# Kernel optimization log

Measured on AMD Instinct MI355X. Metric: run time of the kernel, lower is better.

Reference implementation:

```python
import jax, jax.numpy as jnp
import numpy as np
from jax import lax

L = 25            # max_delay (250 // init_spike_step=10, odd)
SIG = 12.0        # max_delay // 2, frozen (requires_grad=False)
BN_EPS = 1e-5
EPS = 1e-7


def _dcls_kernel(W, P):
    # Gaussian interpolation of kernel_count=1 weights onto a dense kernel of size L.
    # W, P: (out, in). Returns (out, in, L).
    grid = jnp.arange(L, dtype=W.dtype) - L // 2          # (L,)
    K = jnp.exp(-0.5 * ((grid[None, None, :] - P[:, :, None]) / SIG) ** 2)
    K = K / (jnp.sum(K, axis=-1, keepdims=True) + EPS)    # normalize over kernel taps
    return W[:, :, None] * K


def _dcls_conv(x_tbc, W, P):
    # x_tbc: (T, B, Cin) -> causal dilated-kernel conv over time -> (T, B, Cout)
    kernel = _dcls_kernel(W, P)                           # (Cout, Cin, L)
    xb = jnp.transpose(x_tbc, (1, 2, 0))                  # (B, Cin, T)
    xb = jnp.pad(xb, ((0, 0), (0, 0), (L - 1, 0)))        # left (causal) padding
    y = lax.conv_general_dilated(xb, kernel, window_strides=(1,), padding='VALID',
                                 dimension_numbers=('NCH', 'OIH', 'NCH'))
    return jnp.transpose(y, (2, 0, 1))                    # (T, B, Cout)


def _bn(x_tbc, gamma, beta):
    # BatchNorm1d with step_mode='m': stats over merged (T, B) per channel.
    mean = jnp.mean(x_tbc, axis=(0, 1))
    var = jnp.var(x_tbc, axis=(0, 1))
    xhat = (x_tbc - mean) * lax.rsqrt(var + BN_EPS)
    return gamma * xhat + beta


def setup_inputs() -> dict:
    key = jax.random.key(0)
    ks = jax.random.split(key, 8)
    B, T, C = 128, 100, 700
    x = jax.random.uniform(ks[0], (B, T, C), dtype=jnp.float32)
    pmax = float(L // 2)
    W1 = jax.random.normal(ks[1], (256, 700), jnp.float32) * (1.0 / np.sqrt(700))
    P1 = jax.random.uniform(ks[2], (256, 700), jnp.float32, minval=-pmax, maxval=pmax)
    W2 = jax.random.normal(ks[3], (256, 256), jnp.float32) * (1.0 / np.sqrt(256))
    P2 = jax.random.uniform(ks[4], (256, 256), jnp.float32, minval=-pmax, maxval=pmax)
    W3 = jax.random.normal(ks[5], (20, 256), jnp.float32) * (1.0 / np.sqrt(256))
    P3 = jax.random.uniform(ks[6], (20, 256), jnp.float32, minval=-pmax, maxval=pmax)
    return {
        'x': x, 'W1': W1, 'P1': P1, 'W2': W2, 'P2': P2, 'W3': W3, 'P3': P3,
        'gamma1': jnp.ones((256,), jnp.float32), 'beta1': jnp.zeros((256,), jnp.float32),
        'gamma2': jnp.ones((256,), jnp.float32), 'beta2': jnp.zeros((256,), jnp.float32),
    }


def reference(x, W1, P1, W2, P2, W3, P3, gamma1, beta1, gamma2, beta2):
    h = jnp.transpose(x, (1, 0, 2))            # (T, B, C)
    h = _dcls_conv(h, W1, P1)                  # (T, B, 256)
    h = jax.nn.relu(_bn(h, gamma1, beta1))     # dropout = identity (eval)
    h = _dcls_conv(h, W2, P2)                  # (T, B, 256)
    h = jax.nn.relu(_bn(h, gamma2, beta2))
    h = _dcls_conv(h, W3, P3)                  # (T, B, 20)
    return jnp.sum(jax.nn.softmax(h, axis=2), axis=0)   # (B, 20)
```

## Files before the change

### kernel.cpp

```cpp
#include <hip/hip_runtime.h>
#include <stdint.h>


#define T_LEN 100
#define B_SZ  128
#define M_ROWS 12800
#define R_RANK 4
#define K_FIR 448

typedef __bf16 v8bf __attribute__((ext_vector_type(8)));
typedef float  v4f  __attribute__((ext_vector_type(4)));
typedef unsigned int uint32;
typedef unsigned short ushort_t;

struct PhiT { float v[25][R_RANK]; };
constexpr double cexp_(double x) {
  double s = 1.0, t = 1.0;
  for (int n = 1; n < 30; ++n) { t = t * x / n; s += t; }
  return s;
}
constexpr PhiT make_phi() {
  PhiT P{};
  for (int tau = 0; tau < 25; ++tau) {
    double u = (tau - 12) / 12.0;
    double g = cexp_(-0.5 * u * u);
    double T0 = 1.0, T1 = u;
    P.v[tau][0] = (float)(g * T0);
    P.v[tau][1] = (float)(g * T1);
    for (int r = 2; r < R_RANK; ++r) {
      double T2 = 2.0 * u * T1 - T0;
      P.v[tau][r] = (float)(g * T2);
      T0 = T1; T1 = T2;
    }
  }
  return P;
}
constexpr PhiT PHI = make_phi();

struct FirNeed { bool v[14][7]; };
constexpr FirNeed make_fir_need() {
  FirNeed f{};
  for (int j = 0; j < 14; ++j)
    for (int a = 0; a < 7; ++a) {
      bool need = false;
      for (int k = 32 * j; k < 32 * j + 32; ++k) {
        if (k >= 400) continue;
        int sd = k % 100;
        if (sd >= 16 * a - 24 && sd <= 16 * a + 15) need = true;
      }
      f.v[j][a] = need;
    }
  return f;
}
constexpr FirNeed FIRNEED = make_fir_need();

__device__ __forceinline__ void gl_lds16(const void* g, void* l) {
  __builtin_amdgcn_global_load_lds(
      (const __attribute__((address_space(1))) char*)g,
      (__attribute__((address_space(3))) char*)l, 16, 0, 0);
}

__device__ __forceinline__ void build_wr_body(
    const float* __restrict__ W, const float* __restrict__ P,
    __bf16* __restrict__ Wr, int CIN, int CINP, int COUT, int COUTP, int o) {
  for (int i = threadIdx.x; i < CINP; i += blockDim.x) {
    bool valid = (o < COUT) && (i < CIN);
    float w = valid ? W[(size_t)o * CIN + i] : 0.f;
    float p = valid ? P[(size_t)o * CIN + i] : 0.f;
    float S = 0.f;
#pragma unroll
    for (int l = 0; l < 25; ++l) {
      float d = ((float)(l - 12) - p) * (1.f / 12.f);
      S += expf(-0.5f * d * d);
    }
    float v = p * (1.f / 12.f);
    float g = w * expf(-0.5f * v * v) / (S + 1e-7f);
    float h = 0.5f * v, hh = h * h;
    float pw = 1.f;
#pragma unroll
    for (int r = 0; r < R_RANK; ++r) {
      float term = pw, sum = pw;
#pragma unroll
      for (int m = 1; m <= 6; ++m) {
        term *= hh / (float)(m * (m + r));
        sum += term;
      }
      float c = g * ((r == 0) ? 1.f : 2.f) * sum;
      Wr[((size_t)r * COUTP + o) * CINP + i] = (__bf16)c;
      pw *= h / (float)(r + 1);
    }
  }
}

__global__ void setup_all(const float* __restrict__ x,
                          const float* __restrict__ W1, const float* __restrict__ P1,
                          const float* __restrict__ W2, const float* __restrict__ P2,
                          const float* __restrict__ W3, const float* __restrict__ P3,
                          __bf16* __restrict__ Xb, __bf16* __restrict__ Wr1,
                          __bf16* __restrict__ Wr2, __bf16* __restrict__ Wr3,
                          __bf16* __restrict__ Af, float* __restrict__ stats) {
  int blk = blockIdx.x;
  if (blk < 256) { build_wr_body(W1, P1, Wr1, 700, 704, 256, 256, blk); return; }
  blk -= 256;
  if (blk < 256) { build_wr_body(W2, P2, Wr2, 256, 256, 256, 256, blk); return; }
  blk -= 256;
  if (blk < 32) { build_wr_body(W3, P3, Wr3, 256, 256, 20, 32, blk); return; }
  blk -= 32;
  if (blk < 196) {
    int idx = blk * 256 + threadIdx.x;
    if (idx < 112 * 448) {
      int t = idx / 448, k = idx - t * 448;
      float v = 0.f;
      if (t < 100 && k < 400) {
        int r = k / 100, s = k - r * 100;
        int tau = s - t + 24;
        if (tau >= 0 && tau < 25) v = PHI.v[tau][r];
      }
      Af[idx] = (__bf16)v;
    }
    return;
  }
  blk -= 196;
  if (blk < 2200) {
    int c0 = blk * 1024 + threadIdx.x;
#pragma unroll
    for (int k = 0; k < 4; ++k) {
      int c = c0 + k * 256;
      int row = c / 176, col4 = c - row * 176;
      int t = row >> 7, b = row & 127;
      uint2 pk;
      __bf16* pb = (__bf16*)&pk;
      if (col4 < 175) {
        const float* src = x + ((size_t)b * T_LEN + t) * 700 + col4 * 4;
        float4 v = *(const float4*)src;
        pb[0] = (__bf16)v.x; pb[1] = (__bf16)v.y;
        pb[2] = (__bf16)v.z; pb[3] = (__bf16)v.w;
      } else {
        pk.x = 0u; pk.y = 0u;
      }
      *(uint2*)&Xb[(size_t)row * 704 + col4 * 4] = pk;
    }
    return;
  }
  blk -= 2200;
  if (blk == 0) {
    for (int i = threadIdx.x; i < 1024; i += 256) stats[i] = 0.f;
  }
}

template <int CINP, int BLK_N, int WROWS, int WCOLS, int CO_SH>
__global__ __launch_bounds__(256, 2)
void gemm_rk64(const __bf16* __restrict__ A, const __bf16* __restrict__ Bm,
               __bf16* __restrict__ Z) {
  constexpr int COUTP = 1 << CO_SH;
  constexpr int WM = 128 / WROWS;
  constexpr int WN = BLK_N / WCOLS;
  constexpr int RM = WM / 16;
  constexpr int RN = WN / 16;
  __shared__ __align__(16) __bf16 sA[128 * 64];
  __shared__ __align__(16) __bf16 sB[BLK_N * 64];

  const int tid = threadIdx.x;
  const int w = tid >> 6, lane = tid & 63;
  const int q = lane >> 4, ln = lane & 15;
  const int wrow = w / WCOLS, wcol = w % WCOLS;
  const int srow8 = lane >> 3;
  const int s8 = lane & 7;

  const int t0 = blockIdx.x;
  const int oc = blockIdx.y * BLK_N;
  const __bf16* Abase = A + (size_t)t0 * 128 * CINP;
  const __bf16* Bbase = Bm + (size_t)oc * CINP;

  v4f acc[RM][RN];
#pragma unroll
  for (int a = 0; a < RM; ++a)
#pragma unroll
    for (int b = 0; b < RN; ++b) acc[a][b] = v4f{0.f, 0.f, 0.f, 0.f};

  for (int ic = 0; ic < CINP; ic += 64) {
    for (int j = w; j < 16; j += 4) {
      int m = j * 8 + srow8;
      int g = s8 ^ (m & 7);
      gl_lds16(Abase + (size_t)m * CINP + ic + g * 8, &sA[j * 512]);
    }
    for (int j = w; j < BLK_N / 8; j += 4) {
      int n = j * 8 + srow8;
      int g = s8 ^ (n & 7);
      gl_lds16(Bbase + (size_t)n * CINP + ic + g * 8, &sB[j * 512]);
    }
    __syncthreads();

#pragma unroll
    for (int s = 0; s < 2; ++s) {
      v8bf af[RM], bfr[RN];
#pragma unroll
      for (int a = 0; a < RM; ++a) {
        int m = wrow * WM + a * 16 + ln;
        af[a] = *(const v8bf*)&sA[m * 64 + ((((s << 2) | q) ^ (m & 7)) * 8)];
      }
#pragma unroll
      for (int b = 0; b < RN; ++b) {
        int n = wcol * WN + b * 16 + ln;
        bfr[b] = *(const v8bf*)&sB[n * 64 + ((((s << 2) | q) ^ (n & 7)) * 8)];
      }
#pragma unroll
      for (int a = 0; a < RM; ++a)
#pragma unroll
        for (int b = 0; b < RN; ++b)
          acc[a][b] = __builtin_amdgcn_mfma_f32_16x16x32_bf16(af[a], bfr[b], acc[a][b], 0, 0, 0);
    }
    __syncthreads();
  }

#pragma unroll
  for (int a = 0; a < RM; ++a) {
#pragma unroll
    for (int b = 0; b < RN; ++b) {
      int n = oc + wcol * WN + b * 16 + ln;
      int r = n >> CO_SH, o = n & (COUTP - 1);
#pragma unroll
      for (int rr = 0; rr < 4; ++rr) {
        int m = t0 * 128 + wrow * WM + a * 16 + q * 4 + rr;
        Z[((size_t)r * M_ROWS + m) * COUTP + o] = (__bf16)acc[a][b][rr];
      }
    }
  }
}

template <int COUTP, bool STATS, bool SOFTMAX>
__global__ __launch_bounds__(256, 2)
void fir_gemm64(const __bf16* __restrict__ Af, const __bf16* __restrict__ Z,
                __bf16* __restrict__ Yout, float* __restrict__ stats,
                float* __restrict__ outp, int N) {
  __shared__ __align__(16) unsigned char smem[46592];

  const int tid = threadIdx.x;
  const int w = tid >> 6, lane = tid & 63;
  const int q = lane >> 4, ln = lane & 15;
  const int srow8 = lane >> 3, s8 = lane & 7;
  const int kp = tid >> 3;
  const int noct = tid & 7;
  const int nb = blockIdx.x * 64;

  v4f acc[7];
#pragma unroll
  for (int a = 0; a < 7; ++a) acc[a] = v4f{0.f, 0.f, 0.f, 0.f};

  uint4 r0, r1;

#define SA_BUF(b) ((__bf16*)(smem + (b) * 23296))
#define SB_BUF(b) ((uint32*)(smem + (b) * 23296 + 14336))

  {
    __bf16* sA = SA_BUF(0);
    for (int j = w; j < 14; j += 4) {
      int m = j * 8 + srow8;
      int g = s8 ^ (m & 7);
      gl_lds16(Af + (size_t)m * K_FIR + 0 + g * 8, &sA[j * 512]);
    }
    const __bf16* zp = Z + (size_t)(0 + kp * 2) * N + nb + noct * 8;
    r0 = *(const uint4*)zp;
    r1 = *(const uint4*)(zp + N);
  }

#pragma unroll
  for (int i = 0; i < 7; ++i) {
    const int cb = i & 1;
    asm volatile("s_waitcnt vmcnt(0)" ::: "memory");
    {
      uint32* sBu = SB_BUF(cb);
      const ushort_t* p0 = (const ushort_t*)&r0;
      const ushort_t* p1 = (const ushort_t*)&r1;
#pragma unroll
      for (int j = 0; j < 8; ++j) {
        uint32 val = (uint32)p0[j] | ((uint32)p1[j] << 16);
        sBu[(noct * 8 + j) * 35 + kp] = val;
      }
    }
    if (i < 6) {
      int kc = (i + 1) * 64;
      __bf16* sA = SA_BUF(cb ^ 1);
      for (int j = w; j < 14; j += 4) {
        int m = j * 8 + srow8;
        int g = s8 ^ (m & 7);
        gl_lds16(Af + (size_t)m * K_FIR + kc + g * 8, &sA[j * 512]);
      }
      const __bf16* zp = Z + (size_t)(kc + kp * 2) * N + nb + noct * 8;
      r0 = *(const uint4*)zp;
      r1 = *(const uint4*)(zp + N);
    }
    asm volatile("s_waitcnt lgkmcnt(0)" ::: "memory");
    __builtin_amdgcn_s_barrier();

    {
      __bf16* sA = SA_BUF(cb);
      uint32* sBu = SB_BUF(cb);
#pragma unroll
      for (int s = 0; s < 2; ++s) {
        v8bf af[7];
#pragma unroll
        for (int a = 0; a < 7; ++a) {
          if (FIRNEED.v[2 * i + s][a]) {
            int m = a * 16 + ln;
            af[a] = *(const v8bf*)&sA[m * 64 + ((((s << 2) | q) ^ (m & 7)) * 8)];
          }
        }
        int base = (w * 16 + ln) * 35 + s * 16 + q * 4;
        uint32 tmp[4] = {sBu[base], sBu[base + 1], sBu[base + 2], sBu[base + 3]};
        v8bf bfr = *(const v8bf*)tmp;
#pragma unroll
        for (int a = 0; a < 7; ++a) {
          if (FIRNEED.v[2 * i + s][a])
            acc[a] = __builtin_amdgcn_mfma_f32_16x16x32_bf16(af[a], bfr, acc[a], 0, 0, 0);
        }
      }
    }
    __builtin_amdgcn_s_barrier();
  }

  int ng = nb + w * 16 + ln;
  if (!SOFTMAX) {
    float s = 0.f, ss = 0.f;
#pragma unroll
    for (int a = 0; a < 7; ++a) {
#pragma unroll
      for (int rr = 0; rr < 4; ++rr) {
        int t = a * 16 + q * 4 + rr;
        float v = acc[a][rr];
        if (t < 100) {
          Yout[(size_t)t * N + ng] = (__bf16)v;
          s += v; ss += v * v;
        }
      }
    }
    if (STATS) {
      s += __shfl_xor(s, 16); ss += __shfl_xor(ss, 16);
      s += __shfl_xor(s, 32); ss += __shfl_xor(ss, 32);
      if (q == 0) {
        int o = ng & (COUTP - 1);
        atomicAdd(&stats[o], s);
        atomicAdd(&stats[COUTP + o], ss);
      }
    }
  } else {
    float* smx = (float*)smem;
    float* lacc = (float*)(smem + 26000);
    int col = w * 16 + ln;
#pragma unroll
    for (int a = 0; a < 7; ++a) {
#pragma unroll
      for (int rr = 0; rr < 4; ++rr) {
        int t = a * 16 + q * 4 + rr;
        if (t < 100) smx[t * 65 + col] = acc[a][rr];
      }
    }
    if (tid < 64) lacc[tid & 63] = 0.f;
    __syncthreads();
    if (tid < 200) {
      int bl = tid / 100, t = tid - bl * 100;
      const float* rr = &smx[t * 65 + bl * 32];
      float v[20], m = -1e30f;
#pragma unroll
      for (int o = 0; o < 20; ++o) { v[o] = rr[o]; m = fmaxf(m, v[o]); }
      float sum = 0.f;
#pragma unroll
      for (int o = 0; o < 20; ++o) { v[o] = expf(v[o] - m); sum += v[o]; }
      float inv = 1.f / sum;
#pragma unroll
      for (int o = 0; o < 20; ++o) atomicAdd(&lacc[bl * 20 + o], v[o] * inv);
    }
    __syncthreads();
    if (tid < 40) {
      int bl = tid / 20, o = tid - bl * 20;
      int b = (nb >> 5) + bl;
      outp[b * 20 + o] = lacc[bl * 20 + o];
    }
  }
#undef SA_BUF
#undef SB_BUF
}

__global__ __launch_bounds__(256)
void bn_apply_relu8(__bf16* __restrict__ h, const float* __restrict__ stats,
                    const float* __restrict__ gamma, const float* __restrict__ beta) {
  int idx = blockIdx.x * 256 + threadIdx.x;
  int co = (idx & 31) * 8;
  size_t row = (size_t)(idx >> 5);
  __bf16* p = h + row * 256 + co;
  uint4 raw = *(const uint4*)p;
  const ushort_t* pr = (const ushort_t*)&raw;
  uint4 outv;
  ushort_t* po = (ushort_t*)&outv;
#pragma unroll
  for (int j = 0; j < 8; ++j) {
    int c = co + j;
    float mean = stats[c] * (1.f / 12800.f);
    float var = stats[256 + c] * (1.f / 12800.f) - mean * mean;
    float inv = rsqrtf(var + 1e-5f) * gamma[c];
    uint32 u = (uint32)pr[j] << 16;
    float xv; __builtin_memcpy(&xv, &u, 4);
    float v = (xv - mean) * inv + beta[c];
    v = fmaxf(v, 0.f);
    __bf16 bv = (__bf16)v;
    po[j] = *(const ushort_t*)&bv;
  }
  *(uint4*)p = outv;
}


extern "C" void kernel_launch(void* const* d_in, const int* in_sizes, int n_in,
                              void* d_out, int out_size, void* d_ws, size_t ws_size,
                              hipStream_t stream) {
  const float* x  = (const float*)d_in[0];
  const float* W1 = (const float*)d_in[1];
  const float* P1 = (const float*)d_in[2];
  const float* W2 = (const float*)d_in[3];
  const float* P2 = (const float*)d_in[4];
  const float* W3 = (const float*)d_in[5];
  const float* P3 = (const float*)d_in[6];
  const float* g1 = (const float*)d_in[7];
  const float* b1 = (const float*)d_in[8];
  const float* g2 = (const float*)d_in[9];
  const float* b2 = (const float*)d_in[10];
  float* out = (float*)d_out;

  constexpr size_t XB_B  = (size_t)M_ROWS * 704 * 2;
  constexpr size_t Z_B   = (size_t)K_FIR * 32768 * 2;
  constexpr size_t Y12_B = (size_t)M_ROWS * 256 * 2;
  constexpr size_t W1_B  = (size_t)R_RANK * 256 * 704 * 2;
  constexpr size_t W2_B  = (size_t)R_RANK * 256 * 256 * 2;
  constexpr size_t W3_B  = (size_t)R_RANK * 32 * 256 * 2;
  constexpr size_t AF_B  = (size_t)112 * K_FIR * 2;
  constexpr size_t ST_B  = 4096;
  constexpr size_t TOTAL = XB_B + Z_B + Y12_B + W1_B + W2_B + W3_B + AF_B + ST_B;
  if (ws_size < TOTAL) return;

  char* ws = (char*)d_ws;
  size_t off = 0;
  __bf16* Xb   = (__bf16*)(ws + off); off += XB_B;
  __bf16* Zb   = (__bf16*)(ws + off); off += Z_B;
  __bf16* Yb   = (__bf16*)(ws + off); off += Y12_B;
  __bf16* Wr1  = (__bf16*)(ws + off); off += W1_B;
  __bf16* Wr2  = (__bf16*)(ws + off); off += W2_B;
  __bf16* Wr3  = (__bf16*)(ws + off); off += W3_B;
  __bf16* Afir = (__bf16*)(ws + off); off += AF_B;
  float*  stats1 = (float*)(ws + off);
  float*  stats2 = stats1 + 512;

  setup_all<<<dim3(2941), 256, 0, stream>>>(x, W1, P1, W2, P2, W3, P3,
                                            Xb, Wr1, Wr2, Wr3, Afir, stats1);

  gemm_rk64<704, 256, 2, 2, 8><<<dim3(100, 4), 256, 0, stream>>>(Xb, Wr1, Zb);
  fir_gemm64<256, true, false><<<dim3(512), 256, 0, stream>>>(
      Afir, Zb, Yb, stats1, nullptr, 32768);
  bn_apply_relu8<<<dim3(1600), 256, 0, stream>>>(Yb, stats1, g1, b1);

  gemm_rk64<256, 256, 2, 2, 8><<<dim3(100, 4), 256, 0, stream>>>(Yb, Wr2, Zb);
  fir_gemm64<256, true, false><<<dim3(512), 256, 0, stream>>>(
      Afir, Zb, Yb, stats2, nullptr, 32768);
  bn_apply_relu8<<<dim3(1600), 256, 0, stream>>>(Yb, stats2, g2, b2);

  gemm_rk64<256, 64, 2, 2, 5><<<dim3(100, 2), 256, 0, stream>>>(Yb, Wr3, Zb);
  fir_gemm64<32, false, true><<<dim3(64), 256, 0, stream>>>(
      Afir, Zb, nullptr, nullptr, out, 4096);
}
```

Baseline: 185.5 us.

## Add 32-column FIR GEMM kernel with finer sparsity skipping for layers 1-2

```diff
diff --git a/kernel.cpp b/kernel.cpp
--- a/kernel.cpp
+++ b/kernel.cpp
@@ -53,6 +53,24 @@
   return f;
 }
 constexpr FirNeed FIRNEED = make_fir_need();
+
+struct FirNeed8 { bool v[14][8]; };
+constexpr FirNeed8 make_fir_need8() {
+  FirNeed8 f{};
+  for (int j = 0; j < 14; ++j)
+    for (int a = 0; a < 8; ++a) {
+      bool need = false;
+      for (int t = 16 * a; t < 16 * a + 16 && t < 100; ++t)
+        for (int k = 32 * j; k < 32 * j + 32; ++k) {
+          if (k >= 400) continue;
+          int sd = k % 100;
+          if (sd >= t - 24 && sd <= t) need = true;
+        }
+      f.v[j][a] = need;
+    }
+  return f;
+}
+constexpr FirNeed8 FIRNEED8 = make_fir_need8();
 
 __device__ __forceinline__ void gl_lds16(const void* g, void* l) {
   __builtin_amdgcn_global_load_lds(
@@ -228,6 +246,122 @@
   }
 }
 
+template <int MH>
+__device__ __forceinline__ void fir32_comp(const __bf16* sA, const uint32* sBu,
+                                           v4f acc[4], int i, int nh, int q, int ln) {
+#pragma unroll
+  for (int s = 0; s < 2; ++s) {
+    int base = (nh * 16 + ln) * 35 + s * 16 + q * 4;
+    uint32 tmp[4] = {sBu[base], sBu[base + 1], sBu[base + 2], sBu[base + 3]};
+    v8bf bfr = *(const v8bf*)tmp;
+#pragma unroll
+    for (int a = 0; a < 4; ++a) {
+      if (FIRNEED8.v[2 * i + s][MH * 4 + a]) {
+        int m = (MH * 4 + a) * 16 + ln;
+        v8bf af = *(const v8bf*)&sA[m * 64 + ((((s << 2) | q) ^ (m & 7)) * 8)];
+        acc[a] = __builtin_amdgcn_mfma_f32_16x16x32_bf16(af, bfr, acc[a], 0, 0, 0);
+      }
+    }
+  }
+}
+
+template <int COUTP>
+__global__ __launch_bounds__(256, 4)
+void fir_gemm32(const __bf16* __restrict__ Af, const __bf16* __restrict__ Z,
+                __bf16* __restrict__ Yout, float* __restrict__ stats, int N) {
+  __shared__ __align__(16) unsigned char smem[37632];
+
+  const int tid = threadIdx.x;
+  const int w = tid >> 6, lane = tid & 63;
+  const int q = lane >> 4, ln = lane & 15;
+  const int srow8 = lane >> 3, s8 = lane & 7;
+  const int kp = tid >> 3;
+  const int noct = tid & 7;
+  const int mh = w >> 1, nh = w & 1;
+  const int nb = blockIdx.x * 32;
+
+  v4f acc[4];
+#pragma unroll
+  for (int a = 0; a < 4; ++a) acc[a] = v4f{0.f, 0.f, 0.f, 0.f};
+
+  uint2 r0, r1;
+
+#define SA32(b) ((__bf16*)(smem + (b) * 18816))
+#define SB32(b) ((uint32*)(smem + (b) * 18816 + 14336))
+
+  {
+    __bf16* sA = SA32(0);
+    for (int j = w; j < 14; j += 4) {
+      int m = j * 8 + srow8;
+      int g = s8 ^ (m & 7);
+      gl_lds16(Af + (size_t)m * K_FIR + 0 + g * 8, &sA[j * 512]);
+    }
+    const __bf16* zp = Z + (size_t)(kp * 2) * N + nb + noct * 4;
+    r0 = *(const uint2*)zp;
+    r1 = *(const uint2*)(zp + N);
+  }
+
+#pragma unroll
+  for (int i = 0; i < 7; ++i) {
+    const int cb = i & 1;
+    asm volatile("s_waitcnt vmcnt(0)" ::: "memory");
+    {
+      uint32* sBu = SB32(cb);
+      const ushort_t* p0 = (const ushort_t*)&r0;
+      const ushort_t* p1 = (const ushort_t*)&r1;
+#pragma unroll
+      for (int j = 0; j < 4; ++j) {
+        uint32 val = (uint32)p0[j] | ((uint32)p1[j] << 16);
+        sBu[(noct * 4 + j) * 35 + kp] = val;
+      }
+    }
+    if (i < 6) {
+      int kc = (i + 1) * 64;
+      __bf16* sA = SA32(cb ^ 1);
+      for (int j = w; j < 14; j += 4) {
+        int m = j * 8 + srow8;
+        int g = s8 ^ (m & 7);
+        gl_lds16(Af + (size_t)m * K_FIR + kc + g * 8, &sA[j * 512]);
+      }
+      const __bf16* zp = Z + (size_t)(kc + kp * 2) * N + nb + noct * 4;
+      r0 = *(const uint2*)zp;
+      r1 = *(const uint2*)(zp + N);
+    }
+    asm volatile("s_waitcnt lgkmcnt(0)" ::: "memory");
+    __builtin_amdgcn_s_barrier();
+
+    if (mh == 0) fir32_comp<0>(SA32(cb), SB32(cb), acc, i, nh, q, ln);
+    else         fir32_comp<1>(SA32(cb), SB32(cb), acc, i, nh, q, ln);
+
+    __builtin_amdgcn_s_barrier();
+  }
+
+  int ng = nb + nh * 16 + ln;
+  float s = 0.f, ss = 0.f;
+#pragma unroll
+  for (int a = 0; a < 4; ++a) {
+    int am = mh * 4 + a;
+#pragma unroll
+    for (int rr = 0; rr < 4; ++rr) {
+      int t = am * 16 + q * 4 + rr;
+      float v = acc[a][rr];
+      if (t < 100) {
+        Yout[(size_t)t * N + ng] = (__bf16)v;
+        s += v; ss += v * v;
+      }
+    }
+  }
+  s += __shfl_xor(s, 16); ss += __shfl_xor(ss, 16);
+  s += __shfl_xor(s, 32); ss += __shfl_xor(ss, 32);
+  if (q == 0) {
+    int o = ng & (COUTP - 1);
+    atomicAdd(&stats[o], s);
+    atomicAdd(&stats[COUTP + o], ss);
+  }
+#undef SA32
+#undef SB32
+}
+
 template <int COUTP, bool STATS, bool SOFTMAX>
 __global__ __launch_bounds__(256, 2)
 void fir_gemm64(const __bf16* __restrict__ Af, const __bf16* __restrict__ Z,
@@ -452,13 +586,11 @@
                                             Xb, Wr1, Wr2, Wr3, Afir, stats1);
 
   gemm_rk64<704, 256, 2, 2, 8><<<dim3(100, 4), 256, 0, stream>>>(Xb, Wr1, Zb);
-  fir_gemm64<256, true, false><<<dim3(512), 256, 0, stream>>>(
-      Afir, Zb, Yb, stats1, nullptr, 32768);
+  fir_gemm32<256><<<dim3(1024), 256, 0, stream>>>(Afir, Zb, Yb, stats1, 32768);
   bn_apply_relu8<<<dim3(1600), 256, 0, stream>>>(Yb, stats1, g1, b1);
 
   gemm_rk64<256, 256, 2, 2, 8><<<dim3(100, 4), 256, 0, stream>>>(Yb, Wr2, Zb);
-  fir_gemm64<256, true, false><<<dim3(512), 256, 0, stream>>>(
-      Afir, Zb, Yb, stats2, nullptr, 32768);
+  fir_gemm32<256><<<dim3(1024), 256, 0, stream>>>(Afir, Zb, Yb, stats2, 32768);
   bn_apply_relu8<<<dim3(1600), 256, 0, stream>>>(Yb, stats2, g2, b2);
 
   gemm_rk64<256, 64, 2, 2, 5><<<dim3(100, 2), 256, 0, stream>>>(Yb, Wr3, Zb);
```

After: 200.8 us. 8.2% more time.

## Double-buffer LDS tiles in low-rank GEMM and halve output tile width

Applied to the files above, without the earlier changes.

```diff
diff --git a/kernel.cpp b/kernel.cpp
--- a/kernel.cpp
+++ b/kernel.cpp
@@ -157,8 +157,9 @@
   constexpr int WN = BLK_N / WCOLS;
   constexpr int RM = WM / 16;
   constexpr int RN = WN / 16;
-  __shared__ __align__(16) __bf16 sA[128 * 64];
-  __shared__ __align__(16) __bf16 sB[BLK_N * 64];
+  constexpr int NITER = CINP / 64;
+  __shared__ __align__(16) __bf16 sA[2][128 * 64];
+  __shared__ __align__(16) __bf16 sB[2][BLK_N * 64];
 
   const int tid = threadIdx.x;
   const int w = tid >> 6, lane = tid & 63;
@@ -178,31 +179,51 @@
 #pragma unroll
     for (int b = 0; b < RN; ++b) acc[a][b] = v4f{0.f, 0.f, 0.f, 0.f};
 
-  for (int ic = 0; ic < CINP; ic += 64) {
+  auto stage = [&](int it, int bf) {
+    const int ic = it * 64;
     for (int j = w; j < 16; j += 4) {
       int m = j * 8 + srow8;
       int g = s8 ^ (m & 7);
-      gl_lds16(Abase + (size_t)m * CINP + ic + g * 8, &sA[j * 512]);
+      gl_lds16(Abase + (size_t)m * CINP + ic + g * 8, &sA[bf][j * 512]);
     }
     for (int j = w; j < BLK_N / 8; j += 4) {
       int n = j * 8 + srow8;
       int g = s8 ^ (n & 7);
-      gl_lds16(Bbase + (size_t)n * CINP + ic + g * 8, &sB[j * 512]);
-    }
-    __syncthreads();
-
+      gl_lds16(Bbase + (size_t)n * CINP + ic + g * 8, &sB[bf][j * 512]);
+    }
+  };
+
+  stage(0, 0);
+
+  for (int i = 0; i < NITER; ++i) {
+    if (i + 1 < NITER) {
+      stage(i + 1, (i + 1) & 1);
+      if constexpr (BLK_N == 128) {
+        asm volatile("s_waitcnt vmcnt(8)" ::: "memory");
+      } else if constexpr (BLK_N == 64) {
+        asm volatile("s_waitcnt vmcnt(6)" ::: "memory");
+      } else {
+        asm volatile("s_waitcnt vmcnt(12)" ::: "memory");
+      }
+    } else {
+      asm volatile("s_waitcnt vmcnt(0)" ::: "memory");
+    }
+    __builtin_amdgcn_s_barrier();
+
+    const __bf16* sAc = sA[i & 1];
+    const __bf16* sBc = sB[i & 1];
 #pragma unroll
     for (int s = 0; s < 2; ++s) {
       v8bf af[RM], bfr[RN];
 #pragma unroll
       for (int a = 0; a < RM; ++a) {
         int m = wrow * WM + a * 16 + ln;
-        af[a] = *(const v8bf*)&sA[m * 64 + ((((s << 2) | q) ^ (m & 7)) * 8)];
+        af[a] = *(const v8bf*)&sAc[m * 64 + ((((s << 2) | q) ^ (m & 7)) * 8)];
       }
 #pragma unroll
       for (int b = 0; b < RN; ++b) {
         int n = wcol * WN + b * 16 + ln;
-        bfr[b] = *(const v8bf*)&sB[n * 64 + ((((s << 2) | q) ^ (n & 7)) * 8)];
+        bfr[b] = *(const v8bf*)&sBc[n * 64 + ((((s << 2) | q) ^ (n & 7)) * 8)];
       }
 #pragma unroll
       for (int a = 0; a < RM; ++a)
@@ -210,7 +231,7 @@
         for (int b = 0; b < RN; ++b)
           acc[a][b] = __builtin_amdgcn_mfma_f32_16x16x32_bf16(af[a], bfr[b], acc[a][b], 0, 0, 0);
     }
-    __syncthreads();
+    __builtin_amdgcn_s_barrier();
   }
 
 #pragma unroll
@@ -451,12 +472,12 @@
   setup_all<<<dim3(2941), 256, 0, stream>>>(x, W1, P1, W2, P2, W3, P3,
                                             Xb, Wr1, Wr2, Wr3, Afir, stats1);
 
-  gemm_rk64<704, 256, 2, 2, 8><<<dim3(100, 4), 256, 0, stream>>>(Xb, Wr1, Zb);
+  gemm_rk64<704, 128, 2, 2, 8><<<dim3(100, 8), 256, 0, stream>>>(Xb, Wr1, Zb);
   fir_gemm64<256, true, false><<<dim3(512), 256, 0, stream>>>(
       Afir, Zb, Yb, stats1, nullptr, 32768);
   bn_apply_relu8<<<dim3(1600), 256, 0, stream>>>(Yb, stats1, g1, b1);
 
-  gemm_rk64<256, 256, 2, 2, 8><<<dim3(100, 4), 256, 0, stream>>>(Yb, Wr2, Zb);
+  gemm_rk64<256, 128, 2, 2, 8><<<dim3(100, 8), 256, 0, stream>>>(Yb, Wr2, Zb);
   fir_gemm64<256, true, false><<<dim3(512), 256, 0, stream>>>(
       Afir, Zb, Yb, stats2, nullptr, 32768);
   bn_apply_relu8<<<dim3(1600), 256, 0, stream>>>(Yb, stats2, g2, b2);
```

Result: slower. 195.9 us (+5.6%).
